# Performance work log

Measured on AMD Instinct MI355X. Metric: run time of the kernel, lower is better.

## Reference

```python
import jax, jax.numpy as jnp
import numpy as np

B, S, D = 4, 2048, 2048
H, G, HD = 16, 4, 128  # num_heads, kv groups, head_dim
THETA = 10000.0


def setup_inputs() -> dict:
    key = jax.random.key(0)
    ks = jax.random.split(key, 5)
    sc_in = 1.0 / np.sqrt(D)
    sc_out = 1.0 / np.sqrt(H * HD)
    return {
        "x": jax.random.normal(ks[0], (B, S, D), jnp.float32),
        "Wq": jax.random.normal(ks[1], (D, H, HD), jnp.float32) * sc_in,
        "bq": jnp.zeros((H, HD), jnp.float32),
        "Wk": jax.random.normal(ks[2], (D, G, HD), jnp.float32) * sc_in,
        "bk": jnp.zeros((G, HD), jnp.float32),
        "Wv": jax.random.normal(ks[3], (D, G, HD), jnp.float32) * sc_in,
        "bv": jnp.zeros((G, HD), jnp.float32),
        "Wo": jax.random.normal(ks[4], (H, HD, D), jnp.float32) * sc_out,
        "bo": jnp.zeros((D,), jnp.float32),
    }


def _rope(q, k):
    # q: [B,S,H,HD], k: [B,S,G,HD]; LLaMA-style rotate-half RoPE
    half = HD // 2
    inv_freq = 1.0 / (THETA ** (jnp.arange(0, HD, 2, dtype=jnp.float32) / HD))  # [half]
    ang = jnp.arange(S, dtype=jnp.float32)[:, None] * inv_freq  # [S, half]
    cos = jnp.cos(ang)[None, :, None, :]  # [1,S,1,half]
    sin = jnp.sin(ang)[None, :, None, :]

    def rot(t):
        t1, t2 = t[..., :half], t[..., half:]
        return jnp.concatenate([t1 * cos - t2 * sin, t2 * cos + t1 * sin], axis=-1)

    return rot(q), rot(k)


def reference(x, Wq, bq, Wk, bk, Wv, bv, Wo, bo):
    q = jnp.einsum("bsd,dhk->bshk", x, Wq) + bq  # [B,S,H,HD]
    k = jnp.einsum("bsd,dgk->bsgk", x, Wk) + bk  # [B,S,G,HD]
    v = jnp.einsum("bsd,dgk->bsgk", x, Wv) + bv
    q, k = _rope(q, k)
    # replicate_for_multi_query: repeat kv heads to num_heads
    k = jnp.repeat(k, H // G, axis=-2)  # [B,S,H,HD]
    v = jnp.repeat(v, H // G, axis=-2)
    scale = 1.0 / jnp.sqrt(jnp.asarray(HD, q.dtype))
    scores = jnp.einsum("bqhd,bkhd->bhqk", q * scale, k)  # [B,H,S,S]
    causal = jnp.tril(jnp.ones((S, S), bool))
    scores = jnp.where(causal[None, None], scores, jnp.finfo(scores.dtype).min)
    w = jax.nn.softmax(scores, axis=-1)
    attn = jnp.einsum("bhqk,bkhd->bqhd", w, v)  # [B,S,H,HD]
    return jnp.einsum("bqhd,hdo->bqo", attn, Wo) + bo
```

## Files before the change

### kernel.cpp

```cpp
#include <hip/hip_runtime.h>
#include <hip/hip_bf16.h>
#include <math.h>

#define B_  4
#define S_  2048
#define D_  2048
#define H_  16
#define G_  4
#define HD_ 128

typedef __attribute__((ext_vector_type(8))) short short8;
typedef __attribute__((ext_vector_type(4))) float floatx4;

__device__ __forceinline__ short f2bf(float f) {
    unsigned u = __float_as_uint(f);
    unsigned r = (u + 0x7fff + ((u >> 16) & 1)) >> 16;
    return (short)r;
}
__device__ __forceinline__ float b2f(short s) {
    return __uint_as_float(((unsigned)(unsigned short)s) << 16);
}
__device__ __forceinline__ unsigned pk2(float a, float b) {
    unsigned ua = (__float_as_uint(a) + 0x8000u) >> 16;
    unsigned ub = (__float_as_uint(b) + 0x8000u) & 0xffff0000u;
    return ua | ub;
}
__device__ __forceinline__ unsigned pkr(float a, float b) {
    return (unsigned)(unsigned short)f2bf(a) |
           ((unsigned)(unsigned short)f2bf(b) << 16);
}

#define GLL16(gp, lp) __builtin_amdgcn_global_load_lds( \
    (const __attribute__((address_space(1))) void*)(gp), \
    (__attribute__((address_space(3))) void*)(lp), 16, 0, 0)

__global__ void cvt_bf16_kernel(const float* __restrict__ in,
                                short* __restrict__ out, int n8)
{
    int t = blockIdx.x * 256 + threadIdx.x;
    if (t >= n8) return;
    const float4* p = (const float4*)in + (size_t)t * 2;
    float4 a = p[0], b = p[1];
    short8 r;
    r[0] = f2bf(a.x); r[1] = f2bf(a.y); r[2] = f2bf(a.z); r[3] = f2bf(a.w);
    r[4] = f2bf(b.x); r[5] = f2bf(b.y); r[6] = f2bf(b.z); r[7] = f2bf(b.w);
    ((short8*)out)[t] = r;
}

__global__ __launch_bounds__(256) void tr_bf16_kernel(
    const float* __restrict__ in, short* __restrict__ out, int K, int N)
{
    __shared__ float T[32][33];
    int n0 = blockIdx.x * 32, k0 = blockIdx.y * 32;
    int tx = threadIdx.x & 31, ty = threadIdx.x >> 5;
#pragma unroll
    for (int i = 0; i < 4; ++i)
        T[ty + i * 8][tx] = in[(size_t)(k0 + ty + i * 8) * N + n0 + tx];
    __syncthreads();
#pragma unroll
    for (int i = 0; i < 4; ++i)
        out[(size_t)(n0 + ty + i * 8) * K + k0 + tx] = f2bf(T[tx][ty + i * 8]);
}

__global__ __launch_bounds__(256) void gemm_qkv(
    const short* __restrict__ A, const short* __restrict__ Bt,
    const float* __restrict__ bq, const float* __restrict__ bk,
    const float* __restrict__ bv, short* __restrict__ qout,
    short* __restrict__ kout, short* __restrict__ vout, int M, int N, int K)
{
    __shared__ short As[128 * 32];
    __shared__ short Bs[128 * 32];
    const int tid = threadIdx.x;
    const int w = tid >> 6, l15 = tid & 15, quad = (tid & 63) >> 4;
    const int wm = w >> 1, wn = w & 1;
    const int m0 = blockIdx.y * 128, n0 = blockIdx.x * 128;

    floatx4 acc[4][4];
#pragma unroll
    for (int i = 0; i < 4; ++i)
#pragma unroll
        for (int j = 0; j < 4; ++j) acc[i][j] = (floatx4){0.f, 0.f, 0.f, 0.f};

    const int arow = tid >> 2, akc = tid & 3;
    const short* Ag0 = A + (size_t)(m0 + arow) * K + akc * 8;
    const short* Ag1 = A + (size_t)(m0 + 64 + arow) * K + akc * 8;
    const short* Bg0 = Bt + (size_t)(n0 + arow) * K + akc * 8;
    const short* Bg1 = Bt + (size_t)(n0 + 64 + arow) * K + akc * 8;
    short* AsW0 = As + (w * 64) * 8;
    short* AsW1 = As + (256 + w * 64) * 8;
    short* BsW0 = Bs + (w * 64) * 8;
    short* BsW1 = Bs + (256 + w * 64) * 8;

    for (int k0 = 0; k0 < K; k0 += 32) {
        GLL16(Ag0 + k0, AsW0);
        GLL16(Ag1 + k0, AsW1);
        GLL16(Bg0 + k0, BsW0);
        GLL16(Bg1 + k0, BsW1);
        __syncthreads();
        short8 af[4], bfr[4];
#pragma unroll
        for (int mt = 0; mt < 4; ++mt)
            af[mt] = *(const short8*)(As + (wm * 64 + mt * 16 + l15) * 32 + quad * 8);
#pragma unroll
        for (int nt = 0; nt < 4; ++nt)
            bfr[nt] = *(const short8*)(Bs + (wn * 64 + nt * 16 + l15) * 32 + quad * 8);
#pragma unroll
        for (int mt = 0; mt < 4; ++mt)
#pragma unroll
            for (int nt = 0; nt < 4; ++nt)
                acc[mt][nt] = __builtin_amdgcn_mfma_f32_16x16x32_bf16(
                    af[mt], bfr[nt], acc[mt][nt], 0, 0, 0);
        __syncthreads();
    }

#pragma unroll
    for (int nt = 0; nt < 4; ++nt) {
        int gcol = n0 + wn * 64 + nt * 16 + l15;
        float bvv = (gcol < 2048) ? bq[gcol]
                  : (gcol < 2560) ? bk[gcol - 2048] : bv[gcol - 2560];
#pragma unroll
        for (int mt = 0; mt < 4; ++mt) {
            int grow = m0 + wm * 64 + mt * 16 + quad * 4;
            floatx4 v = acc[mt][nt];
            if (n0 < 2048) {
#pragma unroll
                for (int r = 0; r < 4; ++r)
                    qout[(size_t)(grow + r) * 2048 + gcol] = f2bf(v[r] + bvv);
            } else if (n0 < 2560) {
                int c = gcol - 2048;
#pragma unroll
                for (int r = 0; r < 4; ++r)
                    kout[(size_t)(grow + r) * 512 + c] = f2bf(v[r] + bvv);
            } else {
                int c = gcol - 2560, gg = c >> 7, dv = c & 127;
                int bb = grow >> 11, s = grow & 2047;
                uint2 pk;
                pk.x = pkr(v[0] + bvv, v[1] + bvv);
                pk.y = pkr(v[2] + bvv, v[3] + bvv);
                *(uint2*)&vout[(((size_t)bb * G_ + gg) * HD_ + dv) * S_ + s] = pk;
            }
        }
    }
}

__global__ __launch_bounds__(256) void gemm_nt_f32(
    const short* __restrict__ A, const short* __restrict__ Bt,
    const float* __restrict__ bias, float* __restrict__ C,
    int M, int N, int K)
{
    __shared__ short As[128 * 32];
    __shared__ short Bs[128 * 32];
    const int tid = threadIdx.x;
    const int w = tid >> 6, l15 = tid & 15, quad = (tid & 63) >> 4;
    const int wm = w >> 1, wn = w & 1;
    const int m0 = blockIdx.y * 128, n0 = blockIdx.x * 128;

    floatx4 acc[4][4];
#pragma unroll
    for (int i = 0; i < 4; ++i)
#pragma unroll
        for (int j = 0; j < 4; ++j) acc[i][j] = (floatx4){0.f, 0.f, 0.f, 0.f};

    const int arow = tid >> 2, akc = tid & 3;
    const short* Ag0 = A + (size_t)(m0 + arow) * K + akc * 8;
    const short* Ag1 = A + (size_t)(m0 + 64 + arow) * K + akc * 8;
    const short* Bg0 = Bt + (size_t)(n0 + arow) * K + akc * 8;
    const short* Bg1 = Bt + (size_t)(n0 + 64 + arow) * K + akc * 8;
    short* AsW0 = As + (w * 64) * 8;
    short* AsW1 = As + (256 + w * 64) * 8;
    short* BsW0 = Bs + (w * 64) * 8;
    short* BsW1 = Bs + (256 + w * 64) * 8;

    for (int k0 = 0; k0 < K; k0 += 32) {
        GLL16(Ag0 + k0, AsW0);
        GLL16(Ag1 + k0, AsW1);
        GLL16(Bg0 + k0, BsW0);
        GLL16(Bg1 + k0, BsW1);
        __syncthreads();
        short8 af[4], bfr[4];
#pragma unroll
        for (int mt = 0; mt < 4; ++mt)
            af[mt] = *(const short8*)(As + (wm * 64 + mt * 16 + l15) * 32 + quad * 8);
#pragma unroll
        for (int nt = 0; nt < 4; ++nt)
            bfr[nt] = *(const short8*)(Bs + (wn * 64 + nt * 16 + l15) * 32 + quad * 8);
#pragma unroll
        for (int mt = 0; mt < 4; ++mt)
#pragma unroll
            for (int nt = 0; nt < 4; ++nt)
                acc[mt][nt] = __builtin_amdgcn_mfma_f32_16x16x32_bf16(
                    af[mt], bfr[nt], acc[mt][nt], 0, 0, 0);
        __syncthreads();
    }

#pragma unroll
    for (int nt = 0; nt < 4; ++nt) {
        int gcol = n0 + wn * 64 + nt * 16 + l15;
        float bvv = bias[gcol];
#pragma unroll
        for (int mt = 0; mt < 4; ++mt) {
            int grow = m0 + wm * 64 + mt * 16 + quad * 4;
            floatx4 v = acc[mt][nt];
#pragma unroll
            for (int r = 0; r < 4; ++r)
                C[(size_t)(grow + r) * N + gcol] = v[r] + bvv;
        }
    }
}

__global__ void rope_bf16_kernel(short* __restrict__ p, int nh, float scale,
                                 int total)
{
    int gid = blockIdx.x * 256 + threadIdx.x;
    if (gid >= total) return;
    int i = gid & 63;
    int rest = gid >> 6;
    int head = rest % nh;
    int rest2 = rest / nh;
    int s = rest2 & (S_ - 1);
    int b = rest2 >> 11;
    size_t base = (((size_t)b * S_ + s) * nh + head) * HD_;
    float inv = __expf((float)i * -0.14391156509f);
    float ang = (float)s * inv;
    float sn, cs;
    sincosf(ang, &sn, &cs);
    float t1 = b2f(p[base + i]), t2 = b2f(p[base + 64 + i]);
    p[base + i]      = f2bf((t1 * cs - t2 * sn) * scale);
    p[base + 64 + i] = f2bf((t2 * cs + t1 * sn) * scale);
}

#define PPITCH 72

__global__ __launch_bounds__(256) void attn_mfma2(
    short* __restrict__ qb, const short* __restrict__ kb,
    const short* __restrict__ vt)
{
    __shared__ short Ks[64 * 128];
    __shared__ short Vs[128 * 64];
    __shared__ short Ps[4][32 * PPITCH];

    const int tid = threadIdx.x;
    const int w = tid >> 6, lane = tid & 63, l15 = lane & 15, quad = lane >> 4;
    const int id = (int)blockIdx.x;
    const int j = id >> 6, grp = j >> 2, pos = j & 3;
    const int qi = (grp == 0) ? (15 - pos)
                 : (grp == 1) ? pos
                 : (grp == 2) ? (11 - pos) : (4 + pos);
    const int q0 = qi * 128;
    const int bh = id & 63, b = bh >> 4, h = bh & 15, g = h >> 2;

    const short* qp = qb + ((((size_t)b * S_) + q0 + w * 32 + l15) * H_ + h) * HD_
                      + quad * 8;
    short8 qf[2][4];
#pragma unroll
    for (int qs = 0; qs < 2; ++qs)
#pragma unroll
        for (int c = 0; c < 4; ++c)
            qf[qs][c] = *(const short8*)(qp + qs * 16 * (H_ * HD_) + c * 32);

    floatx4 ot[2][8];
#pragma unroll
    for (int qs = 0; qs < 2; ++qs)
#pragma unroll
        for (int s = 0; s < 8; ++s) ot[qs][s] = (floatx4){0.f, 0.f, 0.f, 0.f};
    float m_i[2] = {-1e30f, -1e30f}, l_i[2] = {0.f, 0.f};

    const int kkey = tid >> 4, kch = tid & 15;
    const int ksrc = kch ^ (kkey & 7);
    const short* kgb = kb + (((size_t)b * S_) * G_ + g) * HD_ + ksrc * 8;
    const int vdv = tid >> 3, vch = tid & 7;
    const int vsrc = vch ^ (vdv & 7);
    const short* vgb = vt + (((size_t)(b * G_ + g)) * HD_ + vdv) * (size_t)S_
                       + vsrc * 8;
    const int sw = l15 & 7;
    short* pw = Ps[w];

    const int nkt = 2 * (qi + 1);
    for (int kt = 0; kt < nkt; ++kt) {
        __syncthreads();
        const short* kg = kgb + (size_t)(kt * 64) * (G_ * HD_);
        const short* vg = vgb + kt * 64;
#pragma unroll
        for (int i = 0; i < 4; ++i)
            GLL16(kg + (size_t)(kkey + 16 * i) * (G_ * HD_),
                  Ks + (w * 64 + 256 * i) * 8);
#pragma unroll
        for (int i = 0; i < 4; ++i)
            GLL16(vg + (size_t)(32 * i) * S_, Vs + (w * 64 + 256 * i) * 8);
        __syncthreads();

        floatx4 sa[2][4];
#pragma unroll
        for (int qs = 0; qs < 2; ++qs)
#pragma unroll
            for (int ks = 0; ks < 4; ++ks) sa[qs][ks] = (floatx4){0.f, 0.f, 0.f, 0.f};
#pragma unroll
        for (int c = 0; c < 4; ++c)
#pragma unroll
            for (int ks = 0; ks < 4; ++ks) {
                short8 kf = *(const short8*)(Ks +
                    ((l15 + 16 * ks) * 16 + ((c * 4 + quad) ^ sw)) * 8);
                sa[0][ks] = __builtin_amdgcn_mfma_f32_16x16x32_bf16(
                    kf, qf[0][c], sa[0][ks], 0, 0, 0);
                sa[1][ks] = __builtin_amdgcn_mfma_f32_16x16x32_bf16(
                    kf, qf[1][c], sa[1][ks], 0, 0, 0);
            }

        const int kbase = kt * 64;
#pragma unroll
        for (int qs = 0; qs < 2; ++qs) {
            const int qrow = q0 + w * 32 + qs * 16 + l15;
            if (kbase + 63 > q0 + w * 32 + qs * 16) {
#pragma unroll
                for (int ks = 0; ks < 4; ++ks)
#pragma unroll
                    for (int r = 0; r < 4; ++r)
                        if (kbase + ks * 16 + quad * 4 + r > qrow)
                            sa[qs][ks][r] = -1e30f;
            }
            float mx = -1e30f;
#pragma unroll
            for (int ks = 0; ks < 4; ++ks)
#pragma unroll
                for (int r = 0; r < 4; ++r) mx = fmaxf(mx, sa[qs][ks][r]);
            mx = fmaxf(mx, __shfl_xor(mx, 16));
            mx = fmaxf(mx, __shfl_xor(mx, 32));
            float mo = m_i[qs];
            if (!__all(mx - mo <= 11.5f)) {
                float mn = fmaxf(mo, mx);
                float al = exp2f(mo - mn);
                m_i[qs] = mn;
                l_i[qs] *= al;
#pragma unroll
                for (int s = 0; s < 8; ++s) {
                    floatx4 o = ot[qs][s];
                    o[0] *= al; o[1] *= al; o[2] *= al; o[3] *= al;
                    ot[qs][s] = o;
                }
                mo = mn;
            }
            float s0 = 0.f, s1 = 0.f, s2 = 0.f, s3 = 0.f;
#pragma unroll
            for (int ks = 0; ks < 4; ++ks) {
                float p0 = exp2f(sa[qs][ks][0] - mo);
                float p1 = exp2f(sa[qs][ks][1] - mo);
                float p2 = exp2f(sa[qs][ks][2] - mo);
                float p3 = exp2f(sa[qs][ks][3] - mo);
                sa[qs][ks][0] = p0; sa[qs][ks][1] = p1;
                sa[qs][ks][2] = p2; sa[qs][ks][3] = p3;
                s0 += p0; s1 += p1; s2 += p2; s3 += p3;
            }
            float sum = (s0 + s1) + (s2 + s3);
            sum += __shfl_xor(sum, 16);
            sum += __shfl_xor(sum, 32);
            l_i[qs] += sum;
            short* pr = pw + (qs * 16 + l15) * PPITCH;
#pragma unroll
            for (int ks = 0; ks < 4; ++ks) {
                uint2 pkv;
                pkv.x = pk2(sa[qs][ks][0], sa[qs][ks][1]);
                pkv.y = pk2(sa[qs][ks][2], sa[qs][ks][3]);
                *(uint2*)(pr + ks * 16 + quad * 4) = pkv;
            }
        }

#pragma unroll
        for (int kc = 0; kc < 2; ++kc) {
            short8 pf0 = *(const short8*)(pw + l15 * PPITCH + kc * 32 + quad * 8);
            short8 pf1 = *(const short8*)(pw + (16 + l15) * PPITCH + kc * 32 + quad * 8);
#pragma unroll
            for (int s = 0; s < 8; ++s) {
                short8 vf = *(const short8*)(Vs +
                    ((l15 + 16 * s) * 8 + ((kc * 4 + quad) ^ sw)) * 8);
                ot[0][s] = __builtin_amdgcn_mfma_f32_16x16x32_bf16(
                    vf, pf0, ot[0][s], 0, 0, 0);
                ot[1][s] = __builtin_amdgcn_mfma_f32_16x16x32_bf16(
                    vf, pf1, ot[1][s], 0, 0, 0);
            }
        }
    }

#pragma unroll
    for (int qs = 0; qs < 2; ++qs) {
        float inv = 1.f / l_i[qs];
        size_t base = ((((size_t)b * S_) + q0 + w * 32 + qs * 16 + l15) * H_ + h)
                      * HD_;
#pragma unroll
        for (int s = 0; s < 8; ++s) {
            uint2 pkv;
            pkv.x = pkr(ot[qs][s][0] * inv, ot[qs][s][1] * inv);
            pkv.y = pkr(ot[qs][s][2] * inv, ot[qs][s][3] * inv);
            *(uint2*)&qb[base + s * 16 + quad * 4] = pkv;
        }
    }
}

extern "C" void kernel_launch(void* const* d_in, const int* in_sizes, int n_in,
                              void* d_out, int out_size, void* d_ws, size_t ws_size,
                              hipStream_t stream)
{
    const float* x  = (const float*)d_in[0];
    const float* Wq = (const float*)d_in[1];
    const float* bq = (const float*)d_in[2];
    const float* Wk = (const float*)d_in[3];
    const float* bk = (const float*)d_in[4];
    const float* Wv = (const float*)d_in[5];
    const float* bv = (const float*)d_in[6];
    const float* Wo = (const float*)d_in[7];
    const float* bo = (const float*)d_in[8];
    float* out = (float*)d_out;

    short* xb  = (short*)d_ws;
    short* Wt  = xb + 16777216;
    short* qb8 = Wt + 6291456;
    short* kb8 = qb8 + 16777216;
    short* vt8 = kb8 + 4194304;

    const int M = B_ * S_;
    dim3 blk(256);

    cvt_bf16_kernel<<<8192, blk, 0, stream>>>(x, xb, 16777216 / 8);
    tr_bf16_kernel<<<dim3(64, 64), blk, 0, stream>>>(Wq, Wt, 2048, 2048);
    tr_bf16_kernel<<<dim3(16, 64), blk, 0, stream>>>(Wk, Wt + (size_t)2048 * 2048, 2048, 512);
    tr_bf16_kernel<<<dim3(16, 64), blk, 0, stream>>>(Wv, Wt + (size_t)2560 * 2048, 2048, 512);

    gemm_qkv<<<dim3(24, 64), blk, 0, stream>>>(xb, Wt, bq, bk, bv,
                                               qb8, kb8, vt8, M, 3072, 2048);

    tr_bf16_kernel<<<dim3(64, 64), blk, 0, stream>>>(Wo, Wt, 2048, 2048);

    const float qscale = 0.12751744417f;
    rope_bf16_kernel<<<32768, blk, 0, stream>>>(qb8, H_, qscale, M * H_ * 64);
    rope_bf16_kernel<<<8192,  blk, 0, stream>>>(kb8, G_, 1.0f,   M * G_ * 64);

    attn_mfma2<<<dim3(1024), blk, 0, stream>>>(qb8, kb8, vt8);

    gemm_nt_f32<<<dim3(16, 64), blk, 0, stream>>>(qb8, Wt, bo, out, M, 2048, 2048);
}
```

Measured before the change: 636.6 us.

## Replace QKV and output GEMMs with double-buffered 256x256 swizzled LDS GEMM

Both projection GEMMs now use one shared kernel with 256x256 tiles, 512 threads, and a K step of 64. The next tile is double-buffered in LDS with async global-to-LDS loads issued inside four compute phases, and an XOR swizzle on LDS columns reduces bank conflicts. It also raises MFMA priority during compute and waits with vmcnt-based barriers instead of full syncs. This targets the exposed load latency and low arithmetic intensity of the old 128x128 single-buffered GEMMs, but uses 128KB of LDS and many accumulator registers, which can limit occupancy and leaves fewer blocks to fill the machine.

```diff
diff --git a/kernel.cpp b/kernel.cpp
--- a/kernel.cpp
+++ b/kernel.cpp
@@ -62,150 +62,139 @@
         out[(size_t)(n0 + ty + i * 8) * K + k0 + tx] = f2bf(T[tx][ty + i * 8]);
 }
 
-__global__ __launch_bounds__(256) void gemm_qkv(
+__global__ __launch_bounds__(512, 2) void gemm256_8ph(
     const short* __restrict__ A, const short* __restrict__ Bt,
-    const float* __restrict__ bq, const float* __restrict__ bk,
-    const float* __restrict__ bv, short* __restrict__ qout,
-    short* __restrict__ kout, short* __restrict__ vout, int M, int N, int K)
-{
-    __shared__ short As[128 * 32];
-    __shared__ short Bs[128 * 32];
+    int M, int N, int K, int qkvmode,
+    const float* __restrict__ b0, const float* __restrict__ b1,
+    const float* __restrict__ b2, float* __restrict__ Cf,
+    short* __restrict__ qo, short* __restrict__ ko, short* __restrict__ vo)
+{
+    __shared__ short L[65536];
     const int tid = threadIdx.x;
-    const int w = tid >> 6, l15 = tid & 15, quad = (tid & 63) >> 4;
-    const int wm = w >> 1, wn = w & 1;
-    const int m0 = blockIdx.y * 128, n0 = blockIdx.x * 128;
-
-    floatx4 acc[4][4];
-#pragma unroll
-    for (int i = 0; i < 4; ++i)
-#pragma unroll
-        for (int j = 0; j < 4; ++j) acc[i][j] = (floatx4){0.f, 0.f, 0.f, 0.f};
-
-    const int arow = tid >> 2, akc = tid & 3;
-    const short* Ag0 = A + (size_t)(m0 + arow) * K + akc * 8;
-    const short* Ag1 = A + (size_t)(m0 + 64 + arow) * K + akc * 8;
-    const short* Bg0 = Bt + (size_t)(n0 + arow) * K + akc * 8;
-    const short* Bg1 = Bt + (size_t)(n0 + 64 + arow) * K + akc * 8;
-    short* AsW0 = As + (w * 64) * 8;
-    short* AsW1 = As + (256 + w * 64) * 8;
-    short* BsW0 = Bs + (w * 64) * 8;
-    short* BsW1 = Bs + (256 + w * 64) * 8;
-
-    for (int k0 = 0; k0 < K; k0 += 32) {
-        GLL16(Ag0 + k0, AsW0);
-        GLL16(Ag1 + k0, AsW1);
-        GLL16(Bg0 + k0, BsW0);
-        GLL16(Bg1 + k0, BsW1);
-        __syncthreads();
-        short8 af[4], bfr[4];
-#pragma unroll
-        for (int mt = 0; mt < 4; ++mt)
-            af[mt] = *(const short8*)(As + (wm * 64 + mt * 16 + l15) * 32 + quad * 8);
-#pragma unroll
-        for (int nt = 0; nt < 4; ++nt)
-            bfr[nt] = *(const short8*)(Bs + (wn * 64 + nt * 16 + l15) * 32 + quad * 8);
-#pragma unroll
-        for (int mt = 0; mt < 4; ++mt)
-#pragma unroll
-            for (int nt = 0; nt < 4; ++nt)
-                acc[mt][nt] = __builtin_amdgcn_mfma_f32_16x16x32_bf16(
-                    af[mt], bfr[nt], acc[mt][nt], 0, 0, 0);
-        __syncthreads();
+    const int w = tid >> 6, lane = tid & 63, l15 = lane & 15, quad = lane >> 4;
+    const int wm = w >> 2, wn = w & 3;
+    const int n0 = blockIdx.x * 256, m0 = blockIdx.y * 256;
+    const int NT = K >> 6;
+
+    const int srow = tid >> 2;
+    const int gch8 = ((tid & 3) ^ (srow & 3)) * 8;
+    const int csw8 = (quad ^ (l15 & 3)) * 8;
+
+    floatx4 acc[8][4];
+#pragma unroll
+    for (int f = 0; f < 8; ++f)
+#pragma unroll
+        for (int g = 0; g < 4; ++g) acc[f][g] = (floatx4){0.f, 0.f, 0.f, 0.f};
+
+    const short* Ab = A  + (size_t)(m0 + srow) * K + gch8;
+    const short* Bb = Bt + (size_t)(n0 + srow) * K + gch8;
+    const size_t rj = (size_t)128 * K;
+
+#define STGA(tt, KH, DB) do { \
+    const short* s_ = Ab + (size_t)(tt) * 64 + (KH) * 32; \
+    short* d_ = L + (DB) * 32768 + (KH) * 8192 + tid * 8; \
+    GLL16(s_, d_); GLL16(s_ + rj, d_ + 4096); } while (0)
+#define STGB(tt, KH, DB) do { \
+    const short* s_ = Bb + (size_t)(tt) * 64 + (KH) * 32; \
+    short* d_ = L + (DB) * 32768 + 16384 + (KH) * 8192 + tid * 8; \
+    GLL16(s_, d_); GLL16(s_ + rj, d_ + 4096); } while (0)
+
+    STGA(0, 0, 0); STGB(0, 0, 0); STGA(0, 1, 0); STGB(0, 1, 0);
+    asm volatile("s_waitcnt vmcnt(4)" ::: "memory");
+    asm volatile("s_barrier" ::: "memory");
+
+#define PH(KS, FH, STAGE_STMT) do { \
+    short8 afr[4], bfr[4]; \
+    _Pragma("unroll") \
+    for (int i = 0; i < 4; ++i) \
+        afr[i] = *(const short8*)(ab + (KS) * 8192 + \
+                 (wm * 128 + ((FH) * 4 + i) * 16 + l15) * 32 + csw8); \
+    _Pragma("unroll") \
+    for (int g = 0; g < 4; ++g) \
+        bfr[g] = *(const short8*)(bb + (KS) * 8192 + \
+                 (wn * 64 + g * 16 + l15) * 32 + csw8); \
+    STAGE_STMT; \
+    __builtin_amdgcn_s_setprio(1); \
+    _Pragma("unroll") \
+    for (int i = 0; i < 4; ++i) { \
+        acc[(FH)*4+i][0] = __builtin_amdgcn_mfma_f32_16x16x32_bf16(afr[i], bfr[0], acc[(FH)*4+i][0], 0, 0, 0); \
+        acc[(FH)*4+i][1] = __builtin_amdgcn_mfma_f32_16x16x32_bf16(afr[i], bfr[1], acc[(FH)*4+i][1], 0, 0, 0); \
+        acc[(FH)*4+i][2] = __builtin_amdgcn_mfma_f32_16x16x32_bf16(afr[i], bfr[2], acc[(FH)*4+i][2], 0, 0, 0); \
+        acc[(FH)*4+i][3] = __builtin_amdgcn_mfma_f32_16x16x32_bf16(afr[i], bfr[3], acc[(FH)*4+i][3], 0, 0, 0); \
+    } \
+    __builtin_amdgcn_s_setprio(0); } while (0)
+
+#define PHW \
+    asm volatile("s_waitcnt vmcnt(4)" ::: "memory"); \
+    asm volatile("s_barrier" ::: "memory");
+
+    for (int t = 0; t < NT - 1; ++t) {
+        const int cur = t & 1, nxt = cur ^ 1;
+        const short* ab = L + cur * 32768;
+        const short* bb = ab + 16384;
+        PH(0, 0, STGA(t + 1, 0, nxt)); PHW;
+        PH(0, 1, STGB(t + 1, 0, nxt)); PHW;
+        PH(1, 0, STGA(t + 1, 1, nxt)); PHW;
+        PH(1, 1, STGB(t + 1, 1, nxt)); PHW;
     }
-
-#pragma unroll
-    for (int nt = 0; nt < 4; ++nt) {
-        int gcol = n0 + wn * 64 + nt * 16 + l15;
-        float bvv = (gcol < 2048) ? bq[gcol]
-                  : (gcol < 2560) ? bk[gcol - 2048] : bv[gcol - 2560];
-#pragma unroll
-        for (int mt = 0; mt < 4; ++mt) {
-            int grow = m0 + wm * 64 + mt * 16 + quad * 4;
-            floatx4 v = acc[mt][nt];
-            if (n0 < 2048) {
+    asm volatile("s_waitcnt vmcnt(0)" ::: "memory");
+    asm volatile("s_barrier" ::: "memory");
+    {
+        const int cur = (NT - 1) & 1;
+        const short* ab = L + cur * 32768;
+        const short* bb = ab + 16384;
+        PH(0, 0, (void)0); PH(0, 1, (void)0);
+        PH(1, 0, (void)0); PH(1, 1, (void)0);
+    }
+
+    if (!qkvmode) {
+#pragma unroll
+        for (int f = 0; f < 8; ++f) {
+            int grow = m0 + wm * 128 + f * 16 + quad * 4;
+#pragma unroll
+            for (int g = 0; g < 4; ++g) {
+                int gcol = n0 + wn * 64 + g * 16 + l15;
+                float bvv = b0[gcol];
+                floatx4 v = acc[f][g];
 #pragma unroll
                 for (int r = 0; r < 4; ++r)
-                    qout[(size_t)(grow + r) * 2048 + gcol] = f2bf(v[r] + bvv);
-            } else if (n0 < 2560) {
-                int c = gcol - 2048;
-#pragma unroll
-                for (int r = 0; r < 4; ++r)
-                    kout[(size_t)(grow + r) * 512 + c] = f2bf(v[r] + bvv);
-            } else {
-                int c = gcol - 2560, gg = c >> 7, dv = c & 127;
-                int bb = grow >> 11, s = grow & 2047;
-                uint2 pk;
-                pk.x = pkr(v[0] + bvv, v[1] + bvv);
-                pk.y = pkr(v[2] + bvv, v[3] + bvv);
-                *(uint2*)&vout[(((size_t)bb * G_ + gg) * HD_ + dv) * S_ + s] = pk;
+                    Cf[(size_t)(grow + r) * N + gcol] = v[r] + bvv;
+            }
+        }
+    } else {
+#pragma unroll
+        for (int g = 0; g < 4; ++g) {
+            int gcol = n0 + wn * 64 + g * 16 + l15;
+            float bvv = (gcol < 2048) ? b0[gcol]
+                      : (gcol < 2560) ? b1[gcol - 2048] : b2[gcol - 2560];
+#pragma unroll
+            for (int f = 0; f < 8; ++f) {
+                int grow = m0 + wm * 128 + f * 16 + quad * 4;
+                floatx4 v = acc[f][g];
+                if (n0 < 2048) {
+#pragma unroll
+                    for (int r = 0; r < 4; ++r)
+                        qo[(size_t)(grow + r) * 2048 + gcol] = f2bf(v[r] + bvv);
+                } else if (n0 < 2560) {
+                    int c = gcol - 2048;
+#pragma unroll
+                    for (int r = 0; r < 4; ++r)
+                        ko[(size_t)(grow + r) * 512 + c] = f2bf(v[r] + bvv);
+                } else {
+                    int c = gcol - 2560, gg = c >> 7, dv = c & 127;
+                    int bb2 = grow >> 11, s = grow & 2047;
+                    uint2 pk;
+                    pk.x = pkr(v[0] + bvv, v[1] + bvv);
+                    pk.y = pkr(v[2] + bvv, v[3] + bvv);
+                    *(uint2*)&vo[(((size_t)bb2 * G_ + gg) * HD_ + dv) * S_ + s] = pk;
+                }
             }
         }
     }
-}
-
-__global__ __launch_bounds__(256) void gemm_nt_f32(
-    const short* __restrict__ A, const short* __restrict__ Bt,
-    const float* __restrict__ bias, float* __restrict__ C,
-    int M, int N, int K)
-{
-    __shared__ short As[128 * 32];
-    __shared__ short Bs[128 * 32];
-    const int tid = threadIdx.x;
-    const int w = tid >> 6, l15 = tid & 15, quad = (tid & 63) >> 4;
-    const int wm = w >> 1, wn = w & 1;
-    const int m0 = blockIdx.y * 128, n0 = blockIdx.x * 128;
-
-    floatx4 acc[4][4];
-#pragma unroll
-    for (int i = 0; i < 4; ++i)
-#pragma unroll
-        for (int j = 0; j < 4; ++j) acc[i][j] = (floatx4){0.f, 0.f, 0.f, 0.f};
-
-    const int arow = tid >> 2, akc = tid & 3;
-    const short* Ag0 = A + (size_t)(m0 + arow) * K + akc * 8;
-    const short* Ag1 = A + (size_t)(m0 + 64 + arow) * K + akc * 8;
-    const short* Bg0 = Bt + (size_t)(n0 + arow) * K + akc * 8;
-    const short* Bg1 = Bt + (size_t)(n0 + 64 + arow) * K + akc * 8;
-    short* AsW0 = As + (w * 64) * 8;
-    short* AsW1 = As + (256 + w * 64) * 8;
-    short* BsW0 = Bs + (w * 64) * 8;
-    short* BsW1 = Bs + (256 + w * 64) * 8;
-
-    for (int k0 = 0; k0 < K; k0 += 32) {
-        GLL16(Ag0 + k0, AsW0);
-        GLL16(Ag1 + k0, AsW1);
-        GLL16(Bg0 + k0, BsW0);
-        GLL16(Bg1 + k0, BsW1);
-        __syncthreads();
-        short8 af[4], bfr[4];
-#pragma unroll
-        for (int mt = 0; mt < 4; ++mt)
-            af[mt] = *(const short8*)(As + (wm * 64 + mt * 16 + l15) * 32 + quad * 8);
-#pragma unroll
-        for (int nt = 0; nt < 4; ++nt)
-            bfr[nt] = *(const short8*)(Bs + (wn * 64 + nt * 16 + l15) * 32 + quad * 8);
-#pragma unroll
-        for (int mt = 0; mt < 4; ++mt)
-#pragma unroll
-            for (int nt = 0; nt < 4; ++nt)
-                acc[mt][nt] = __builtin_amdgcn_mfma_f32_16x16x32_bf16(
-                    af[mt], bfr[nt], acc[mt][nt], 0, 0, 0);
-        __syncthreads();
-    }
-
-#pragma unroll
-    for (int nt = 0; nt < 4; ++nt) {
-        int gcol = n0 + wn * 64 + nt * 16 + l15;
-        float bvv = bias[gcol];
-#pragma unroll
-        for (int mt = 0; mt < 4; ++mt) {
-            int grow = m0 + wm * 64 + mt * 16 + quad * 4;
-            floatx4 v = acc[mt][nt];
-#pragma unroll
-            for (int r = 0; r < 4; ++r)
-                C[(size_t)(grow + r) * N + gcol] = v[r] + bvv;
-        }
-    }
+#undef PH
+#undef PHW
+#undef STGA
+#undef STGB
 }
 
 __global__ void rope_bf16_kernel(short* __restrict__ p, int nh, float scale,
@@ -424,8 +413,8 @@
     tr_bf16_kernel<<<dim3(16, 64), blk, 0, stream>>>(Wk, Wt + (size_t)2048 * 2048, 2048, 512);
     tr_bf16_kernel<<<dim3(16, 64), blk, 0, stream>>>(Wv, Wt + (size_t)2560 * 2048, 2048, 512);
 
-    gemm_qkv<<<dim3(24, 64), blk, 0, stream>>>(xb, Wt, bq, bk, bv,
-                                               qb8, kb8, vt8, M, 3072, 2048);
+    gemm256_8ph<<<dim3(12, 32), dim3(512), 0, stream>>>(
+        xb, Wt, M, 3072, 2048, 1, bq, bk, bv, nullptr, qb8, kb8, vt8);
 
     tr_bf16_kernel<<<dim3(64, 64), blk, 0, stream>>>(Wo, Wt, 2048, 2048);
 
@@ -435,5 +424,7 @@
 
     attn_mfma2<<<dim3(1024), blk, 0, stream>>>(qb8, kb8, vt8);
 
-    gemm_nt_f32<<<dim3(16, 64), blk, 0, stream>>>(qb8, Wt, bo, out, M, 2048, 2048);
-}
+    gemm256_8ph<<<dim3(8, 32), dim3(512), 0, stream>>>(
+        qb8, Wt, M, 2048, 2048, 0, bo, nullptr, nullptr, out,
+        nullptr, nullptr, nullptr);
+}
```

Result: faster. 591.9 us (-7.0%).
